# Optimization experiments

Hardware: AMD Instinct MI355X
Metric: run time of the kernel (lower is better)

Reference implementation:

```python
import jax, jax.numpy as jnp
import numpy as np

B, P, K = 8, 8192, 16          # batches, points per batch, knn neighbors
CHANNELS = [4, 32, 64]          # input_channels + NUM_FILTERS
EPS = 1e-5                      # BatchNorm1d eps


def setup_inputs() -> dict:
    key = jax.random.key(0)
    ks = jax.random.split(key, 16)
    N = B * P
    pillar_features = jax.random.normal(ks[0], (N, CHANNELS[0]), jnp.float32)
    pos = jax.random.uniform(ks[1], (N, 3), jnp.float32) * 50.0
    batch_idx = jnp.repeat(jnp.arange(B, dtype=jnp.float32), P)
    voxel_coords = jnp.concatenate([batch_idx[:, None], pos], axis=1)  # [N,4]
    inp = {"pillar_features": pillar_features, "voxel_coords": voxel_coords}
    j = 2
    for i in range(len(CHANNELS) - 1):
        cin, cout = CHANNELS[i], CHANNELS[i + 1]
        inp[f"W{i}"] = jax.random.normal(ks[j], (cout, 2 * cin), jnp.float32) / np.sqrt(2 * cin); j += 1
        inp[f"b{i}"] = jnp.zeros((cout,), jnp.float32)
        inp[f"gamma{i}"] = jnp.ones((cout,), jnp.float32)
        inp[f"beta{i}"] = jnp.zeros((cout,), jnp.float32)
        inp[f"wk{i}"] = jax.random.normal(ks[j], (cout,), jnp.float32) / np.sqrt(cout); j += 1
        inp[f"wq{i}"] = jax.random.normal(ks[j], (cout,), jnp.float32) / np.sqrt(cout); j += 1
    return inp


def _knn(pos):
    # pos: [N,3]; equal-sized batches of P points (batch_idx = repeat(arange(B), P))
    pb = pos.reshape(B, P, 3)
    def per_batch(p):  # p: [P,3]
        d = jnp.sum((p[:, None, :] - p[None, :, :]) ** 2, axis=-1)  # [P,P]
        _, idx = jax.lax.top_k(-d, K)                               # k nearest (incl. self)
        return idx
    idx = jax.lax.map(per_batch, pb)                                # [B,P,K], one PxP at a time
    return (idx + (jnp.arange(B) * P)[:, None, None]).reshape(B * P, K)


def _edgeconv(x, idx, pos, W, b, gamma, beta, wk, wq):
    # x: [N,F], idx: [N,K] int, pos: [N,3]
    xi = x[:, None, :]                                  # [N,1,F]
    xj = x[idx]                                         # [N,K,F] gather
    e = jnp.concatenate([jnp.broadcast_to(xi, xj.shape), xj - xi], axis=-1)  # [N,K,2F]
    h = jnp.einsum('nke,oe->nok', e, W) + b[None, :, None]  # 1x1 Conv1d -> [N,O,K]
    h = jax.nn.relu(h)
    # BatchNorm1d (training-mode stats over N and K per channel, biased var)
    mu = jnp.mean(h, axis=(0, 2), keepdims=True)
    var = jnp.mean(jnp.square(h - mu), axis=(0, 2), keepdims=True)
    h = (h - mu) * jax.lax.rsqrt(var + EPS) * gamma[None, :, None] + beta[None, :, None]
    # attention: K^T Q -> [N,K,K], softmax over dim 1, feature @ att
    Kv = jnp.einsum('nok,o->nk', h, wk)
    Qv = jnp.einsum('nok,o->nk', h, wq)
    att = jax.nn.softmax(Kv[:, :, None] * Qv[:, None, :], axis=1)  # [N,K,K]
    h = jnp.einsum('nok,nkq->noq', h, att)
    # distance-based sigmoid scaling then max over neighbors
    vec = pos[idx] - pos[:, None, :]                    # [N,K,3]
    dis = jnp.sqrt(jnp.sum(vec * vec, axis=-1))         # [N,K]
    scale = 2.0 * jax.nn.sigmoid(-dis)                  # [N,K]
    return jnp.max(scale[:, None, :] * h, axis=-1)      # [N,O]


def reference(pillar_features, voxel_coords,
              W0, b0, gamma0, beta0, wk0, wq0,
              W1, b1, gamma1, beta1, wk1, wq1):
    pos = voxel_coords[:, 1:4]
    idx = _knn(jax.lax.stop_gradient(pos))  # torch knn is under no_grad
    x = pillar_features                      # [N,4]
    x = _edgeconv(x, idx, pos, W0, b0, gamma0, beta0, wk0, wq0)
    x = _edgeconv(x, idx, pos, W1, b1, gamma1, beta1, wk1, wq1)
    return (x, voxel_coords)
```

## Files before the change

kernel.cpp:

```cpp
#include <hip/hip_runtime.h>
#include <math.h>

#define B_ 8
#define P_ 8192
#define N_ 65536
#define K_ 16
#define EPS_ 1e-5f
#define NBK 1024
#define BSCALE 20.48f

__global__ __launch_bounds__(256) void init_bins(int* counts, int* cursors,
                                                 int* xminI, int* xmaxI) {
    int i = blockIdx.x * 256 + threadIdx.x;
    counts[i] = 0; cursors[i] = 0;
    xminI[i] = 0x7F7FFFFF;
    xmaxI[i] = 0x80000000;
}

__device__ __forceinline__ int bucket_of(float x) {
    int b = (int)(x * BSCALE);
    return b > (NBK - 1) ? (NBK - 1) : (b < 0 ? 0 : b);
}

__global__ __launch_bounds__(256) void count_kernel(const float* __restrict__ vc,
                                                    int* counts, int* xminI, int* xmaxI) {
    int q = blockIdx.x * 256 + threadIdx.x;
    float4 p = ((const float4*)vc)[q];
    int b = q >> 13;
    int bk = bucket_of(p.y);
    int e = b * NBK + bk;
    atomicAdd(&counts[e], 1);
    int xb = __float_as_int(p.y);
    atomicMin(&xminI[e], xb);
    atomicMax(&xmaxI[e], xb);
}

__global__ __launch_bounds__(1024) void scan_kernel(const int* __restrict__ counts,
                                                    const int* __restrict__ xminI,
                                                    const int* __restrict__ xmaxI,
                                                    int* off, float* xlub, float* xglb) {
    __shared__ int   smi[NBK];
    __shared__ float smf[NBK];
    int b = blockIdx.x, t = threadIdx.x;
    int e = b * NBK + t;

    int c = counts[e];
    smi[t] = c; __syncthreads();
    for (int s = 1; s < NBK; s <<= 1) {
        int u = smi[t]; int v = (t >= s) ? smi[t - s] : 0;
        __syncthreads(); smi[t] = u + v; __syncthreads();
    }
    off[b * (NBK + 1) + t] = smi[t] - c;
    if (t == NBK - 1) off[b * (NBK + 1) + NBK] = smi[t];

    float mx = c ? __int_as_float(xmaxI[e]) : -1e30f;
    smf[t] = mx; __syncthreads();
    for (int s = 1; s < NBK; s <<= 1) {
        float u = smf[t]; float v = (t >= s) ? smf[t - s] : -1e30f;
        __syncthreads(); smf[t] = fmaxf(u, v); __syncthreads();
    }
    xlub[e] = smf[t];
    __syncthreads();

    int r = NBK - 1 - t;
    int cr_ = counts[b * NBK + r];
    float mn = cr_ ? __int_as_float(xminI[b * NBK + r]) : 1e30f;
    smf[t] = mn; __syncthreads();
    for (int s = 1; s < NBK; s <<= 1) {
        float u = smf[t]; float v = (t >= s) ? smf[t - s] : 1e30f;
        __syncthreads(); smf[t] = fminf(u, v); __syncthreads();
    }
    xglb[b * NBK + r] = smf[t];
}

__global__ __launch_bounds__(256) void scatter_kernel(const float* __restrict__ vc,
                                                      const int* __restrict__ off,
                                                      int* cursors, float4* pos4s) {
    int q = blockIdx.x * 256 + threadIdx.x;
    float4 p = ((const float4*)vc)[q];
    int b = q >> 13;
    int bk = bucket_of(p.y);
    int slot = off[b * (NBK + 1) + bk] + atomicAdd(&cursors[b * NBK + bk], 1);
    pos4s[(b << 13) + slot] = make_float4(p.y, p.z, p.w, __int_as_float(q));
}

__global__ __launch_bounds__(256, 4) void knn3_kernel(const float4* __restrict__ pos4s,
                                                   const float* __restrict__ xlub,
                                                   const float* __restrict__ xglb,
                                                   unsigned short* __restrict__ idx_out,
                                                   float* __restrict__ d2_out) {
    const int tid   = threadIdx.x;
    const int sub   = tid & 3;
    const int bb    = blockIdx.x >> 7;
    const int bbase = bb << 13;
    const int wq    = blockIdx.x & 127;
    const int home0 = bbase + ((wq >> 2) << 8);
    const int qslot = bbase + (wq << 6) + (tid >> 2);
    const float4 me = pos4s[qslot];
    const float qx = me.x, qy = me.y, qz = me.z;
    const int q = __float_as_int(me.w);
    const float* xl = xlub + (bb << 10);
    const float* xg = xglb + (bb << 10);

    __shared__ __align__(16) float4 tile[256];
    __shared__ int sflags[2];

    const double KINF = __longlong_as_double(0x7F800000LL << 16);
    double bd[16];
#pragma unroll
    for (int t = 0; t < 16; ++t) bd[t] = KINF;
    float bd15f = __builtin_huge_valf();
    float sbdf  = __builtin_huge_valf();

    auto CLEAN16 = [](double* m) {
#pragma unroll
        for (int dd = 8; dd >= 1; dd >>= 1)
#pragma unroll
            for (int i = 0; i < 16; ++i)
                if ((i & dd) == 0) {
                    double lo = fmin(m[i], m[i | dd]);
                    m[i | dd] = fmax(m[i], m[i | dd]);
                    m[i] = lo;
                }
    };

    auto QUAD16K = [&]() -> double {
        double m[16];
#pragma unroll
        for (int i = 0; i < 16; ++i)
            m[i] = fmin(bd[i], __shfl_xor(bd[15 - i], 1, 64));
        CLEAN16(m);
        double t = 0.0;
#pragma unroll
        for (int i = 0; i < 16; ++i)
            t = fmax(t, fmin(m[i], __shfl_xor(m[15 - i], 2, 64)));
        return t;
    };

#define DIST_(c)                                                            \
    float dx = __fsub_rn(qx, (c).x);                                        \
    float dy = __fsub_rn(qy, (c).y);                                        \
    float dz = __fsub_rn(qz, (c).z);                                        \
    float d  = __fadd_rn(__fadd_rn(__fmul_rn(dx,dx), __fmul_rn(dy,dy)),     \
                         __fmul_rn(dz,dz));

#define SCAN_(base, cntT) {                                                 \
    __syncthreads();                                                        \
    if (tid < (cntT)) tile[tid] = pos4s[(base) + tid];                      \
    __syncthreads();                                                        \
    float g_ = fminf(bd15f, sbdf);                                          \
    _Pragma("unroll 4")                                                     \
    for (int j = sub; j < (cntT); j += 4) {                                 \
        float4 c = tile[j];                                                 \
        DIST_(c)                                                            \
        if (d <= g_) {                                                      \
            double key = __longlong_as_double(                              \
                ((long long)((unsigned long long)__float_as_uint(d) << 16)) \
                | (long long)(unsigned long long)((unsigned)__float_as_int(c.w) & 0xFFFFu)); \
            _Pragma("unroll")                                               \
            for (int t = 15; t > 0; --t)                                    \
                bd[t] = fmin(bd[t], fmax(bd[t-1], key));                    \
            bd[0] = fmin(bd[0], key);                                       \
            bd15f = __uint_as_float((unsigned)                              \
                ((unsigned long long)__double_as_longlong(bd[15]) >> 16));  \
            g_ = fminf(bd15f, sbdf);                                        \
        }                                                                   \
    } }

    SCAN_(home0, 256)
    int sL = home0, sR = home0 + 256;
    for (;;) {
        double sk = QUAD16K();
        sbdf = __uint_as_float((unsigned)
            ((unsigned long long)__double_as_longlong(sk) >> 16));
        bool needL = false, needR = false;
        if (sL > bbase) {
            float xb = xl[bucket_of(pos4s[sL - 1].x)];
            float t = __fsub_rn(qx, xb);
            needL = __fmul_rn(t, t) <= sbdf;
        }
        if (sR < bbase + P_) {
            float xb = xg[bucket_of(pos4s[sR].x)];
            float t = __fsub_rn(xb, qx);
            needR = __fmul_rn(t, t) <= sbdf;
        }
        if (tid == 0) { sflags[0] = 0; sflags[1] = 0; }
        __syncthreads();
        if (needL) sflags[0] = 1;
        if (needR) sflags[1] = 1;
        __syncthreads();
        int aL = sflags[0], aR = sflags[1];
        if (!aL && !aR) break;
        if (aL) { int c_ = min(256, sL - bbase);       SCAN_(sL - c_, c_) sL -= c_; }
        if (aR) { int c_ = min(256, bbase + P_ - sR);  SCAN_(sR, c_)      sR += c_; }
    }

    double m[16];
#pragma unroll
    for (int i = 0; i < 16; ++i)
        m[i] = fmin(bd[i], __shfl_xor(bd[15 - i], 1, 64));
    CLEAN16(m);
    double u[16];
#pragma unroll
    for (int i = 0; i < 16; ++i)
        u[i] = fmin(m[i], __shfl_xor(m[15 - i], 2, 64));
    CLEAN16(u);

    if (sub == 0) {
        float4*  d4 = (float4*)(d2_out + (size_t)q * K_);
        ushort4* i4 = (ushort4*)(idx_out + (size_t)q * K_);
#define OUT4(t4, a, b, cc, dd_)                                             \
        { unsigned long long ka = (unsigned long long)__double_as_longlong(u[a]);  \
          unsigned long long kb = (unsigned long long)__double_as_longlong(u[b]);  \
          unsigned long long kc = (unsigned long long)__double_as_longlong(u[cc]); \
          unsigned long long kd = (unsigned long long)__double_as_longlong(u[dd_]);\
          d4[t4] = make_float4(__uint_as_float((unsigned)(ka >> 16)),       \
                               __uint_as_float((unsigned)(kb >> 16)),       \
                               __uint_as_float((unsigned)(kc >> 16)),       \
                               __uint_as_float((unsigned)(kd >> 16)));      \
          i4[t4] = make_ushort4((unsigned short)(ka & 0xFFFFu),             \
                                (unsigned short)(kb & 0xFFFFu),             \
                                (unsigned short)(kc & 0xFFFFu),             \
                                (unsigned short)(kd & 0xFFFFu)); }
        OUT4(0, 0, 1, 2, 3)
        OUT4(1, 4, 5, 6, 7)
        OUT4(2, 8, 9, 10, 11)
        OUT4(3, 12, 13, 14, 15)
#undef OUT4
    }
#undef SCAN_
#undef DIST_
}

template<int CIN, int COUT, bool PHA>
__global__ __launch_bounds__(256) void edge_kernel(
    const float* __restrict__ x,
    const unsigned short* __restrict__ idx,
    const float* __restrict__ d2,
    const float* __restrict__ W,
    const float* __restrict__ bias,
    const float* __restrict__ wk,
    const float* __restrict__ wq,
    const float* __restrict__ acoef,
    const float* __restrict__ ccoef,
    double* __restrict__ gsum,
    double* __restrict__ gsumsq,
    float* __restrict__ out,
    int niter)
{
    constexpr int LOGC = (COUT == 64) ? 6 : 5;
    constexpr int GPW  = 64 / COUT;
    constexpr int GPB  = 4 * GPW;
    constexpr int C4   = CIN / 4;
    constexpr int SJ   = (K_ + 1) * CIN;
    constexpr int HTS  = COUT + 1;
    constexpr int HTN  = PHA ? 1 : (K_ * HTS);
    constexpr int PN   = PHA ? 1 : (K_ * K_);
    constexpr int KQN  = PHA ? 1 : (2 * K_);
    constexpr int SCN  = PHA ? 1 : K_;
    constexpr int WKQN = PHA ? 1 : (2 * COUT);

    const int tid  = threadIdx.x;
    const int wave = tid >> 6;
    const int lane = tid & 63;
    const int lo   = lane & (COUT - 1);
    const int grp  = lane >> LOGC;
    const int gidx = wave * GPW + grp;

    __shared__ __align__(16) float sj_s[GPB][SJ];
    __shared__ __align__(16) float hT_s[GPB][HTN];
    __shared__ __align__(16) float p_s[GPB][PN];
    __shared__ __align__(16) float kqv_s[GPB][KQN];
    __shared__ __align__(16) float rden_s[GPB][SCN];
    __shared__ __align__(16) float scal_s[GPB][SCN];
    __shared__ __align__(16) float wkq_s[WKQN];

    float Wr[CIN], Ad[CIN];
#pragma unroll
    for (int c = 0; c < CIN; ++c) {
        float wl = W[lo * (2*CIN) + c];
        float wr = W[lo * (2*CIN) + CIN + c];
        Wr[c] = wr; Ad[c] = wl - wr;
    }
    const float b_s = bias[lo];

    float a_s = 0.f, c_s = 0.f;
    if constexpr (!PHA) {
        a_s = acoef[lo]; c_s = ccoef[lo];
        if (tid < COUT)            wkq_s[tid] = wk[tid];
        else if (tid < 2*COUT)     wkq_s[tid] = wq[tid - COUT];
        __syncthreads();
    }

    double lsum = 0.0, lsq = 0.0;
    const int g0      = blockIdx.x * GPB + gidx;
    const int gstride = gridDim.x * GPB;

    for (int it = 0; it < niter; ++it) {
        const int n = g0 + it * gstride;

        {
            const float4* xs  = (const float4*)x;
            float4*       sj4 = (float4*)sj_s[gidx];
            constexpr int TOT4 = (K_ + 1) * C4;
#pragma unroll
            for (int e0 = 0; e0 < TOT4; e0 += COUT) {
                int e = e0 + lo;
                if (e < TOT4) {
                    int r = e / C4;
                    int c = e - r * C4;
                    int row = (r < K_) ? (int)idx[n * K_ + r] : n;
                    sj4[e] = xs[row * C4 + c];
                }
            }
        }
        if constexpr (!PHA) {
            if (lo < K_) {
                float dis = sqrtf(d2[n * K_ + lo]);
                float e = __expf(-dis);
                scal_s[gidx][lo] = 2.0f * e / (1.0f + e);
            }
        }
        __builtin_amdgcn_wave_barrier();

        const float* sj = sj_s[gidx];
        float t0 = b_s;
#pragma unroll
        for (int c = 0; c < C4; ++c) {
            float4 v = ((const float4*)(sj + K_ * CIN))[c];
            t0 = fmaf(Ad[4*c  ], v.x, t0);
            t0 = fmaf(Ad[4*c+1], v.y, t0);
            t0 = fmaf(Ad[4*c+2], v.z, t0);
            t0 = fmaf(Ad[4*c+3], v.w, t0);
        }
        float hn[K_];
        float psum = 0.f, psq = 0.f;
#pragma unroll
        for (int k = 0; k < K_; ++k) {
            float acc = t0;
            const float4* xr = (const float4*)(sj + k * CIN);
#pragma unroll
            for (int c = 0; c < C4; ++c) {
                float4 v = xr[c];
                acc = fmaf(Wr[4*c  ], v.x, acc);
                acc = fmaf(Wr[4*c+1], v.y, acc);
                acc = fmaf(Wr[4*c+2], v.z, acc);
                acc = fmaf(Wr[4*c+3], v.w, acc);
            }
            float h = fmaxf(acc, 0.f);
            if constexpr (PHA) {
                psum += h; psq = fmaf(h, h, psq);
            } else {
                hn[k] = fmaf(a_s, h, c_s);
            }
        }
        if constexpr (PHA) {
            lsum += (double)psum;
            lsq  += (double)psq;
        }

        if constexpr (!PHA) {
            float* hT = hT_s[gidx];
#pragma unroll
            for (int k = 0; k < K_; ++k) hT[k * HTS + lo] = hn[k];
            __builtin_amdgcn_wave_barrier();

            const int kk   = lo & 15;
            const int role = lo >> 4;
            float av = 0.f;
            const float* hrow = hT + kk * HTS;
            int obase; const float* wv;
            if constexpr (COUT == 64) { obase = (role & 1) * 32; wv = wkq_s + ((role >> 1) ? COUT : 0); }
            else                      { obase = 0;               wv = wkq_s + (role ? COUT : 0); }
#pragma unroll
            for (int j = 0; j < 32; ++j)
                av = fmaf(hrow[obase + j], wv[obase + j], av);
            if constexpr (COUT == 64) {
                float sum2 = av + __shfl_xor(av, 16, 64);
                if (lo < 16)                  kqv_s[gidx][kk] = sum2;
                else if (lo >= 32 && lo < 48) kqv_s[gidx][16 + kk] = sum2;
            } else {
                kqv_s[gidx][lo] = av;
            }
            __builtin_amdgcn_wave_barrier();

            if (lo < K_) {
                const int qq = lo;
                const float qv = kqv_s[gidx][K_ + qq];
                float m = -__builtin_huge_valf();
#pragma unroll
                for (int k = 0; k < K_; ++k) m = fmaxf(m, kqv_s[gidx][k] * qv);
                float den = 0.f;
#pragma unroll
                for (int k = 0; k < K_; ++k) {
                    float e = __expf(kqv_s[gidx][k] * qv - m);
                    den += e;
                    p_s[gidx][k * K_ + qq] = e;
                }
                rden_s[gidx][qq] = 1.0f / den;
            }
            __builtin_amdgcn_wave_barrier();

            float hq[K_];
#pragma unroll
            for (int qq = 0; qq < K_; ++qq) hq[qq] = 0.f;
#pragma unroll
            for (int k = 0; k < K_; ++k) {
                const float hnk = hn[k];
                const float4* p4 = (const float4*)(p_s[gidx] + k * K_);
#pragma unroll
                for (int j = 0; j < 4; ++j) {
                    float4 v = p4[j];
                    hq[4*j  ] = fmaf(hnk, v.x, hq[4*j  ]);
                    hq[4*j+1] = fmaf(hnk, v.y, hq[4*j+1]);
                    hq[4*j+2] = fmaf(hnk, v.z, hq[4*j+2]);
                    hq[4*j+3] = fmaf(hnk, v.w, hq[4*j+3]);
                }
            }
            float res = -__builtin_huge_valf();
#pragma unroll
            for (int j = 0; j < 4; ++j) {
                float4 sc = ((const float4*)scal_s[gidx])[j];
                float4 rd = ((const float4*)rden_s[gidx])[j];
                res = fmaxf(res, sc.x * (hq[4*j  ] * rd.x));
                res = fmaxf(res, sc.y * (hq[4*j+1] * rd.y));
                res = fmaxf(res, sc.z * (hq[4*j+2] * rd.z));
                res = fmaxf(res, sc.w * (hq[4*j+3] * rd.w));
            }
            out[n * COUT + lo] = res;
            __builtin_amdgcn_wave_barrier();
        } else {
            __builtin_amdgcn_wave_barrier();
        }
    }

    if constexpr (PHA) {
        if constexpr (COUT == 32) {
            long long bs = __double_as_longlong(lsum);
            int l0 = __shfl_xor((int)(bs & 0xffffffffLL), 32, 64);
            int h0 = __shfl_xor((int)(bs >> 32), 32, 64);
            lsum += __longlong_as_double(((long long)h0 << 32) | (unsigned long long)(unsigned int)l0);
            bs = __double_as_longlong(lsq);
            l0 = __shfl_xor((int)(bs & 0xffffffffLL), 32, 64);
            h0 = __shfl_xor((int)(bs >> 32), 32, 64);
            lsq += __longlong_as_double(((long long)h0 << 32) | (unsigned long long)(unsigned int)l0);
        }
        __shared__ double redS[4][COUT];
        __shared__ double redQ[4][COUT];
        if (lane < COUT) { redS[wave][lane] = lsum; redQ[wave][lane] = lsq; }
        __syncthreads();
        if (tid < COUT) {
            double ss = redS[0][tid] + redS[1][tid] + redS[2][tid] + redS[3][tid];
            double qq = redQ[0][tid] + redQ[1][tid] + redQ[2][tid] + redQ[3][tid];
            atomicAdd(&gsum[tid], ss);
            atomicAdd(&gsumsq[tid], qq);
        }
    }
}

__global__ void finalize_kernel(const double* __restrict__ gsum, const double* __restrict__ gsumsq,
                                const float* __restrict__ gamma, const float* __restrict__ beta,
                                float* __restrict__ a, float* __restrict__ c, int cout)
{
    int o = threadIdx.x;
    if (o < cout) {
        const double inv = 1.0 / ((double)N_ * (double)K_);
        double mu  = gsum[o] * inv;
        double var = gsumsq[o] * inv - mu * mu;
        double rs  = 1.0 / sqrt(var + (double)EPS_);
        double av  = rs * (double)gamma[o];
        a[o] = (float)av;
        c[o] = (float)((double)beta[o] - mu * av);
    }
}

__global__ __launch_bounds__(256) void copy_vc(const float4* __restrict__ src,
                                               float4* __restrict__ dst) {
    int i = blockIdx.x * 256 + threadIdx.x;
    dst[i] = src[i];
}

extern "C" void kernel_launch(void* const* d_in, const int* in_sizes, int n_in,
                              void* d_out, int out_size, void* d_ws, size_t ws_size,
                              hipStream_t stream)
{
    const float* pillar = (const float*)d_in[0];
    const float* vc     = (const float*)d_in[1];
    const float* W0  = (const float*)d_in[2];
    const float* b0  = (const float*)d_in[3];
    const float* g0  = (const float*)d_in[4];
    const float* be0 = (const float*)d_in[5];
    const float* wk0 = (const float*)d_in[6];
    const float* wq0 = (const float*)d_in[7];
    const float* W1  = (const float*)d_in[8];
    const float* b1  = (const float*)d_in[9];
    const float* g1  = (const float*)d_in[10];
    const float* be1 = (const float*)d_in[11];
    const float* wk1 = (const float*)d_in[12];
    const float* wq1 = (const float*)d_in[13];

    char* ws = (char*)d_ws;
    double* dsum = (double*)ws;
    double *s0 = dsum, *sq0 = dsum + 64, *s1 = dsum + 128, *sq1 = dsum + 192;
    float* coef = (float*)(ws + 4096);
    float *a0 = coef, *c0 = coef + 64, *a1 = coef + 128, *c1 = coef + 192;
    unsigned short* idx = (unsigned short*)(ws + 8192);
    float* d2  = (float*)(ws + 8192 + (size_t)N_*K_*2);
    float* x1  = (float*)(ws + 8192 + (size_t)N_*K_*6);
    size_t base2 = 8192 + (size_t)N_*K_*6 + (size_t)N_*32*4;
    float4* pos4s = (float4*)(ws + base2);
    int* counts   = (int*)(ws + base2 + (1u<<20));
    int* cursors  = counts + B_*NBK;
    int* off      = cursors + B_*NBK;
    int* xminI    = off + B_*(NBK+1);
    int* xmaxI    = xminI + B_*NBK;
    float* xlub   = (float*)(xmaxI + B_*NBK);
    float* xglb   = xlub + B_*NBK;

    float* xout = (float*)d_out;
    float* vout = xout + (size_t)N_ * 64;

    hipMemsetAsync(dsum, 0, 2048, stream);
    init_bins<<<B_*NBK/256, 256, 0, stream>>>(counts, cursors, xminI, xmaxI);
    count_kernel<<<N_/256, 256, 0, stream>>>(vc, counts, xminI, xmaxI);
    scan_kernel<<<B_, NBK, 0, stream>>>(counts, xminI, xmaxI, off, xlub, xglb);
    scatter_kernel<<<N_/256, 256, 0, stream>>>(vc, off, cursors, pos4s);
    knn3_kernel<<<N_/64, 256, 0, stream>>>(pos4s, xlub, xglb, idx, d2);

    edge_kernel<4,32,true ><<<1024, 256, 0, stream>>>(pillar, idx, d2, W0, b0, wk0, wq0,
                                                      nullptr, nullptr, s0, sq0, nullptr, 8);
    finalize_kernel<<<1, 64, 0, stream>>>(s0, sq0, g0, be0, a0, c0, 32);
    edge_kernel<4,32,false><<<1024, 256, 0, stream>>>(pillar, idx, d2, W0, b0, wk0, wq0,
                                                      a0, c0, nullptr, nullptr, x1, 8);

    edge_kernel<32,64,true ><<<2048, 256, 0, stream>>>(x1, idx, d2, W1, b1, wk1, wq1,
                                                       nullptr, nullptr, s1, sq1, nullptr, 8);
    finalize_kernel<<<1, 64, 0, stream>>>(s1, sq1, g1, be1, a1, c1, 64);
    edge_kernel<32,64,false><<<2048, 256, 0, stream>>>(x1, idx, d2, W1, b1, wk1, wq1,
                                                       a1, c1, nullptr, nullptr, xout, 8);

    copy_vc<<<256, 256, 0, stream>>>((const float4*)vc, (float4*)vout);
}
```

Baseline: 622.3 us.

## Precompute per-point W·x projection for layer 2 and store fp16 distance scales

The second EdgeConv's 1x1 conv is split algebraically into a per-point term (W_left−W_right)·x_i and a per-neighbor term W_right·x_j. The neighbor term is precomputed once per point by a new zgemm kernel, batch by batch into an L2-sized buffer, and then gathered per neighbor. This replaces the 16x redundant 32-wide dot products and the shared-memory staging of neighbor features. The kNN kernel also computes the sigmoid distance scale directly and stores it as fp16 instead of fp32 squared distances, which halves that traffic but loses some precision. The cost is 16 extra kernel launches plus a zgemm that is recomputed in both passes.

```diff
diff --git a/kernel.cpp b/kernel.cpp
--- a/kernel.cpp
+++ b/kernel.cpp
@@ -1,4 +1,5 @@
 #include <hip/hip_runtime.h>
+#include <hip/hip_fp16.h>
 #include <math.h>
 
 #define B_ 8
@@ -88,7 +89,7 @@
                                                    const float* __restrict__ xlub,
                                                    const float* __restrict__ xglb,
                                                    unsigned short* __restrict__ idx_out,
-                                                   float* __restrict__ d2_out) {
+                                                   __half* __restrict__ scal_out) {
     const int tid   = threadIdx.x;
     const int sub   = tid & 3;
     const int bb    = blockIdx.x >> 7;
@@ -207,36 +208,76 @@
     CLEAN16(u);
 
     if (sub == 0) {
-        float4*  d4 = (float4*)(d2_out + (size_t)q * K_);
+        unsigned long long kk[16];
+#pragma unroll
+        for (int t = 0; t < 16; ++t)
+            kk[t] = (unsigned long long)__double_as_longlong(u[t]);
+
         ushort4* i4 = (ushort4*)(idx_out + (size_t)q * K_);
-#define OUT4(t4, a, b, cc, dd_)                                             \
-        { unsigned long long ka = (unsigned long long)__double_as_longlong(u[a]);  \
-          unsigned long long kb = (unsigned long long)__double_as_longlong(u[b]);  \
-          unsigned long long kc = (unsigned long long)__double_as_longlong(u[cc]); \
-          unsigned long long kd = (unsigned long long)__double_as_longlong(u[dd_]);\
-          d4[t4] = make_float4(__uint_as_float((unsigned)(ka >> 16)),       \
-                               __uint_as_float((unsigned)(kb >> 16)),       \
-                               __uint_as_float((unsigned)(kc >> 16)),       \
-                               __uint_as_float((unsigned)(kd >> 16)));      \
-          i4[t4] = make_ushort4((unsigned short)(ka & 0xFFFFu),             \
-                                (unsigned short)(kb & 0xFFFFu),             \
-                                (unsigned short)(kc & 0xFFFFu),             \
-                                (unsigned short)(kd & 0xFFFFu)); }
-        OUT4(0, 0, 1, 2, 3)
-        OUT4(1, 4, 5, 6, 7)
-        OUT4(2, 8, 9, 10, 11)
-        OUT4(3, 12, 13, 14, 15)
-#undef OUT4
+        i4[0] = make_ushort4((unsigned short)(kk[0] & 0xFFFFu), (unsigned short)(kk[1] & 0xFFFFu),
+                             (unsigned short)(kk[2] & 0xFFFFu), (unsigned short)(kk[3] & 0xFFFFu));
+        i4[1] = make_ushort4((unsigned short)(kk[4] & 0xFFFFu), (unsigned short)(kk[5] & 0xFFFFu),
+                             (unsigned short)(kk[6] & 0xFFFFu), (unsigned short)(kk[7] & 0xFFFFu));
+        i4[2] = make_ushort4((unsigned short)(kk[8] & 0xFFFFu), (unsigned short)(kk[9] & 0xFFFFu),
+                             (unsigned short)(kk[10] & 0xFFFFu), (unsigned short)(kk[11] & 0xFFFFu));
+        i4[3] = make_ushort4((unsigned short)(kk[12] & 0xFFFFu), (unsigned short)(kk[13] & 0xFFFFu),
+                             (unsigned short)(kk[14] & 0xFFFFu), (unsigned short)(kk[15] & 0xFFFFu));
+
+        unsigned pw[8];
+#pragma unroll
+        for (int i = 0; i < 8; ++i) {
+            float d0 = __uint_as_float((unsigned)(kk[2*i]     >> 16));
+            float d1 = __uint_as_float((unsigned)(kk[2*i + 1] >> 16));
+            float e0 = __expf(-sqrtf(d0));
+            float e1 = __expf(-sqrtf(d1));
+            float s0 = 2.0f * e0 / (1.0f + e0);
+            float s1 = 2.0f * e1 / (1.0f + e1);
+            pw[i] = (unsigned)__half_as_ushort(__float2half_rn(s0))
+                  | ((unsigned)__half_as_ushort(__float2half_rn(s1)) << 16);
+        }
+        uint4* s4 = (uint4*)(scal_out + (size_t)q * K_);
+        s4[0] = make_uint4(pw[0], pw[1], pw[2], pw[3]);
+        s4[1] = make_uint4(pw[4], pw[5], pw[6], pw[7]);
     }
 #undef SCAN_
 #undef DIST_
 }
 
-template<int CIN, int COUT, bool PHA>
+__global__ __launch_bounds__(256) void zgemm_kernel(const float* __restrict__ x1,
+                                                    const float* __restrict__ W,
+                                                    float* __restrict__ z, int bcur) {
+    const int o  = threadIdx.x & 63;
+    const int pg = threadIdx.x >> 6;
+    float Wr[32];
+    const float4* w4 = (const float4*)(W + o * 64 + 32);
+#pragma unroll
+    for (int c = 0; c < 8; ++c) {
+        float4 v = w4[c];
+        Wr[4*c] = v.x; Wr[4*c+1] = v.y; Wr[4*c+2] = v.z; Wr[4*c+3] = v.w;
+    }
+    const int m0 = blockIdx.x * 16 + pg * 4;
+#pragma unroll
+    for (int i = 0; i < 4; ++i) {
+        const int m = m0 + i;
+        const float4* xr = (const float4*)(x1 + (((size_t)bcur << 13) + m) * 32);
+        float acc = 0.f;
+#pragma unroll
+        for (int c = 0; c < 8; ++c) {
+            float4 v = xr[c];
+            acc = fmaf(Wr[4*c  ], v.x, acc);
+            acc = fmaf(Wr[4*c+1], v.y, acc);
+            acc = fmaf(Wr[4*c+2], v.z, acc);
+            acc = fmaf(Wr[4*c+3], v.w, acc);
+        }
+        z[m * 64 + o] = acc;
+    }
+}
+
+template<int CIN, int COUT, bool PHA, bool USEZ>
 __global__ __launch_bounds__(256) void edge_kernel(
     const float* __restrict__ x,
     const unsigned short* __restrict__ idx,
-    const float* __restrict__ d2,
+    const __half* __restrict__ scal,
     const float* __restrict__ W,
     const float* __restrict__ bias,
     const float* __restrict__ wk,
@@ -246,13 +287,14 @@
     double* __restrict__ gsum,
     double* __restrict__ gsumsq,
     float* __restrict__ out,
-    int niter)
+    const float* __restrict__ zbuf,
+    int bcur, int niter)
 {
     constexpr int LOGC = (COUT == 64) ? 6 : 5;
     constexpr int GPW  = 64 / COUT;
     constexpr int GPB  = 4 * GPW;
     constexpr int C4   = CIN / 4;
-    constexpr int SJ   = (K_ + 1) * CIN;
+    constexpr int SJ   = USEZ ? 4 : ((K_ + 1) * CIN);
     constexpr int HTS  = COUT + 1;
     constexpr int HTN  = PHA ? 1 : (K_ * HTS);
     constexpr int PN   = PHA ? 1 : (K_ * K_);
@@ -275,12 +317,14 @@
     __shared__ __align__(16) float scal_s[GPB][SCN];
     __shared__ __align__(16) float wkq_s[WKQN];
 
-    float Wr[CIN], Ad[CIN];
+    float Ad[CIN];
+    float Wr[USEZ ? 1 : CIN];
 #pragma unroll
     for (int c = 0; c < CIN; ++c) {
         float wl = W[lo * (2*CIN) + c];
         float wr = W[lo * (2*CIN) + CIN + c];
-        Wr[c] = wr; Ad[c] = wl - wr;
+        Ad[c] = wl - wr;
+        if constexpr (!USEZ) Wr[c] = wr;
     }
     const float b_s = bias[lo];
 
@@ -297,63 +341,94 @@
     const int gstride = gridDim.x * GPB;
 
     for (int it = 0; it < niter; ++it) {
-        const int n = g0 + it * gstride;
-
-        {
-            const float4* xs  = (const float4*)x;
-            float4*       sj4 = (float4*)sj_s[gidx];
-            constexpr int TOT4 = (K_ + 1) * C4;
-#pragma unroll
-            for (int e0 = 0; e0 < TOT4; e0 += COUT) {
-                int e = e0 + lo;
-                if (e < TOT4) {
-                    int r = e / C4;
-                    int c = e - r * C4;
-                    int row = (r < K_) ? (int)idx[n * K_ + r] : n;
-                    sj4[e] = xs[row * C4 + c];
-                }
-            }
-        }
-        if constexpr (!PHA) {
-            if (lo < K_) {
-                float dis = sqrtf(d2[n * K_ + lo]);
-                float e = __expf(-dis);
-                scal_s[gidx][lo] = 2.0f * e / (1.0f + e);
-            }
-        }
-        __builtin_amdgcn_wave_barrier();
-
-        const float* sj = sj_s[gidx];
-        float t0 = b_s;
-#pragma unroll
-        for (int c = 0; c < C4; ++c) {
-            float4 v = ((const float4*)(sj + K_ * CIN))[c];
-            t0 = fmaf(Ad[4*c  ], v.x, t0);
-            t0 = fmaf(Ad[4*c+1], v.y, t0);
-            t0 = fmaf(Ad[4*c+2], v.z, t0);
-            t0 = fmaf(Ad[4*c+3], v.w, t0);
-        }
+        const int n = USEZ ? ((bcur << 13) + blockIdx.x * GPB + gidx)
+                           : (g0 + it * gstride);
+
         float hn[K_];
         float psum = 0.f, psq = 0.f;
-#pragma unroll
-        for (int k = 0; k < K_; ++k) {
-            float acc = t0;
-            const float4* xr = (const float4*)(sj + k * CIN);
+
+        if constexpr (USEZ) {
+            float uacc = b_s;
+            const float4* xr = (const float4*)(x + (size_t)n * CIN);
 #pragma unroll
             for (int c = 0; c < C4; ++c) {
                 float4 v = xr[c];
-                acc = fmaf(Wr[4*c  ], v.x, acc);
-                acc = fmaf(Wr[4*c+1], v.y, acc);
-                acc = fmaf(Wr[4*c+2], v.z, acc);
-                acc = fmaf(Wr[4*c+3], v.w, acc);
-            }
-            float h = fmaxf(acc, 0.f);
-            if constexpr (PHA) {
-                psum += h; psq = fmaf(h, h, psq);
-            } else {
-                hn[k] = fmaf(a_s, h, c_s);
-            }
-        }
+                uacc = fmaf(Ad[4*c  ], v.x, uacc);
+                uacc = fmaf(Ad[4*c+1], v.y, uacc);
+                uacc = fmaf(Ad[4*c+2], v.z, uacc);
+                uacc = fmaf(Ad[4*c+3], v.w, uacc);
+            }
+            const uint4* iw = (const uint4*)(idx + (size_t)n * K_);
+            const uint4 ia = iw[0], ib = iw[1];
+            float zk[K_];
+#define GA(k, w, s) { unsigned j = ((w) >> (s)) & 0xFFFFu;                  \
+                      zk[k] = zbuf[(((int)(j & (P_-1))) << LOGC) + lo]; }
+            GA(0,  ia.x, 0) GA(1,  ia.x, 16) GA(2,  ia.y, 0) GA(3,  ia.y, 16)
+            GA(4,  ia.z, 0) GA(5,  ia.z, 16) GA(6,  ia.w, 0) GA(7,  ia.w, 16)
+            GA(8,  ib.x, 0) GA(9,  ib.x, 16) GA(10, ib.y, 0) GA(11, ib.y, 16)
+            GA(12, ib.z, 0) GA(13, ib.z, 16) GA(14, ib.w, 0) GA(15, ib.w, 16)
+#undef GA
+#pragma unroll
+            for (int k = 0; k < K_; ++k) {
+                float h = fmaxf(uacc + zk[k], 0.f);
+                if constexpr (PHA) { psum += h; psq = fmaf(h, h, psq); }
+                else               hn[k] = fmaf(a_s, h, c_s);
+            }
+            if constexpr (!PHA) {
+                if (lo < K_)
+                    scal_s[gidx][lo] = __half2float(scal[(size_t)n * K_ + lo]);
+            }
+            __builtin_amdgcn_wave_barrier();
+        } else {
+            {
+                const float4* xs  = (const float4*)x;
+                float4*       sj4 = (float4*)sj_s[gidx];
+                constexpr int TOT4 = (K_ + 1) * C4;
+#pragma unroll
+                for (int e0 = 0; e0 < TOT4; e0 += COUT) {
+                    int e = e0 + lo;
+                    if (e < TOT4) {
+                        int r = e / C4;
+                        int c = e - r * C4;
+                        int row = (r < K_) ? (int)idx[n * K_ + r] : n;
+                        sj4[e] = xs[row * C4 + c];
+                    }
+                }
+            }
+            if constexpr (!PHA) {
+                if (lo < K_)
+                    scal_s[gidx][lo] = __half2float(scal[(size_t)n * K_ + lo]);
+            }
+            __builtin_amdgcn_wave_barrier();
+
+            const float* sj = sj_s[gidx];
+            float t0 = b_s;
+#pragma unroll
+            for (int c = 0; c < C4; ++c) {
+                float4 v = ((const float4*)(sj + K_ * CIN))[c];
+                t0 = fmaf(Ad[4*c  ], v.x, t0);
+                t0 = fmaf(Ad[4*c+1], v.y, t0);
+                t0 = fmaf(Ad[4*c+2], v.z, t0);
+                t0 = fmaf(Ad[4*c+3], v.w, t0);
+            }
+#pragma unroll
+            for (int k = 0; k < K_; ++k) {
+                float acc = t0;
+                const float4* xrr = (const float4*)(sj + k * CIN);
+#pragma unroll
+                for (int c = 0; c < C4; ++c) {
+                    float4 v = xrr[c];
+                    acc = fmaf(Wr[4*c  ], v.x, acc);
+                    acc = fmaf(Wr[4*c+1], v.y, acc);
+                    acc = fmaf(Wr[4*c+2], v.z, acc);
+                    acc = fmaf(Wr[4*c+3], v.w, acc);
+                }
+                float h = fmaxf(acc, 0.f);
+                if constexpr (PHA) { psum += h; psq = fmaf(h, h, psq); }
+                else               hn[k] = fmaf(a_s, h, c_s);
+            }
+        }
+
         if constexpr (PHA) {
             lsum += (double)psum;
             lsq  += (double)psq;
@@ -387,13 +462,13 @@
             if (lo < K_) {
                 const int qq = lo;
                 const float qv = kqv_s[gidx][K_ + qq];
-                float m = -__builtin_huge_valf();
-#pragma unroll
-                for (int k = 0; k < K_; ++k) m = fmaxf(m, kqv_s[gidx][k] * qv);
+                float mx = -__builtin_huge_valf();
+#pragma unroll
+                for (int k = 0; k < K_; ++k) mx = fmaxf(mx, kqv_s[gidx][k] * qv);
                 float den = 0.f;
 #pragma unroll
                 for (int k = 0; k < K_; ++k) {
-                    float e = __expf(kqv_s[gidx][k] * qv - m);
+                    float e = __expf(kqv_s[gidx][k] * qv - mx);
                     den += e;
                     p_s[gidx][k * K_ + qq] = e;
                 }
@@ -427,7 +502,7 @@
                 res = fmaxf(res, sc.z * (hq[4*j+2] * rd.z));
                 res = fmaxf(res, sc.w * (hq[4*j+3] * rd.w));
             }
-            out[n * COUT + lo] = res;
+            out[(size_t)n * COUT + lo] = res;
             __builtin_amdgcn_wave_barrier();
         } else {
             __builtin_amdgcn_wave_barrier();
@@ -500,14 +575,15 @@
     const float* wq1 = (const float*)d_in[13];
 
     char* ws = (char*)d_ws;
-    double* dsum = (double*)ws;
+    unsigned short* idx = (unsigned short*)ws;
+    __half* scal = (__half*)(ws + (size_t)2*1024*1024);
+    float*  x1   = (float*)(ws + (size_t)4*1024*1024);
+    float*  zbuf = (float*)(ws + (size_t)12*1024*1024);
+    double* dsum = (double*)(ws + 14680064);
     double *s0 = dsum, *sq0 = dsum + 64, *s1 = dsum + 128, *sq1 = dsum + 192;
-    float* coef = (float*)(ws + 4096);
+    float* coef  = (float*)(ws + 14682112);
     float *a0 = coef, *c0 = coef + 64, *a1 = coef + 128, *c1 = coef + 192;
-    unsigned short* idx = (unsigned short*)(ws + 8192);
-    float* d2  = (float*)(ws + 8192 + (size_t)N_*K_*2);
-    float* x1  = (float*)(ws + 8192 + (size_t)N_*K_*6);
-    size_t base2 = 8192 + (size_t)N_*K_*6 + (size_t)N_*32*4;
+    size_t base2 = 14688256;
     float4* pos4s = (float4*)(ws + base2);
     int* counts   = (int*)(ws + base2 + (1u<<20));
     int* cursors  = counts + B_*NBK;
@@ -525,19 +601,29 @@
     count_kernel<<<N_/256, 256, 0, stream>>>(vc, counts, xminI, xmaxI);
     scan_kernel<<<B_, NBK, 0, stream>>>(counts, xminI, xmaxI, off, xlub, xglb);
     scatter_kernel<<<N_/256, 256, 0, stream>>>(vc, off, cursors, pos4s);
-    knn3_kernel<<<N_/64, 256, 0, stream>>>(pos4s, xlub, xglb, idx, d2);
-
-    edge_kernel<4,32,true ><<<1024, 256, 0, stream>>>(pillar, idx, d2, W0, b0, wk0, wq0,
-                                                      nullptr, nullptr, s0, sq0, nullptr, 8);
+    knn3_kernel<<<N_/64, 256, 0, stream>>>(pos4s, xlub, xglb, idx, scal);
+
+    edge_kernel<4,32,true ,false><<<1024, 256, 0, stream>>>(pillar, idx, scal, W0, b0, wk0, wq0,
+                                                            nullptr, nullptr, s0, sq0, nullptr,
+                                                            nullptr, 0, 8);
     finalize_kernel<<<1, 64, 0, stream>>>(s0, sq0, g0, be0, a0, c0, 32);
-    edge_kernel<4,32,false><<<1024, 256, 0, stream>>>(pillar, idx, d2, W0, b0, wk0, wq0,
-                                                      a0, c0, nullptr, nullptr, x1, 8);
-
-    edge_kernel<32,64,true ><<<2048, 256, 0, stream>>>(x1, idx, d2, W1, b1, wk1, wq1,
-                                                       nullptr, nullptr, s1, sq1, nullptr, 8);
+    edge_kernel<4,32,false,false><<<1024, 256, 0, stream>>>(pillar, idx, scal, W0, b0, wk0, wq0,
+                                                            a0, c0, nullptr, nullptr, x1,
+                                                            nullptr, 0, 8);
+
+    for (int b = 0; b < B_; ++b) {
+        zgemm_kernel<<<512, 256, 0, stream>>>(x1, W1, zbuf, b);
+        edge_kernel<32,64,true ,true><<<2048, 256, 0, stream>>>(x1, idx, scal, W1, b1, wk1, wq1,
+                                                                nullptr, nullptr, s1, sq1, nullptr,
+                                                                zbuf, b, 1);
+    }
     finalize_kernel<<<1, 64, 0, stream>>>(s1, sq1, g1, be1, a1, c1, 64);
-    edge_kernel<32,64,false><<<2048, 256, 0, stream>>>(x1, idx, d2, W1, b1, wk1, wq1,
-                                                       a1, c1, nullptr, nullptr, xout, 8);
+    for (int b = 0; b < B_; ++b) {
+        zgemm_kernel<<<512, 256, 0, stream>>>(x1, W1, zbuf, b);
+        edge_kernel<32,64,false,true><<<2048, 256, 0, stream>>>(x1, idx, scal, W1, b1, wk1, wq1,
+                                                                a1, c1, nullptr, nullptr, xout,
+                                                                zbuf, b, 1);
+    }
 
     copy_vc<<<256, 256, 0, stream>>>((const float4*)vc, (float4*)vout);
 }
```

Result: slower. 1.232 ms (+98.0%).
